# Kernel optimization log

Hardware: AMD Instinct MI355X
Metric: run time of the kernel (lower is better)

The kernel has to match this reference:

```python
import jax, jax.numpy as jnp
import numpy as np


def setup_inputs() -> dict:
    key = jax.random.key(0)
    k1, k2, k3 = jax.random.split(key, 3)
    V, B, L = 512, 256, 40
    seq = jax.random.randint(k1, (B, L), 0, V, dtype=jnp.int32)
    sim_mat = jax.random.normal(k2, (V, V), dtype=jnp.float32)
    pers_mat = jax.random.normal(k3, (V, V, V), dtype=jnp.float32)
    weights = jnp.ones((2,), dtype=jnp.float32)
    return {"seq": seq, "sim_mat": sim_mat, "pers_mat": pers_mat, "weights": weights}


def reference(seq, sim_mat, pers_mat, weights):
    # seq: [B, L] int indices into the V unique responses
    B, L = seq.shape
    V = sim_mat.shape[0]
    # Step 0: uniform log_softmax over V ones -> nll = log(V) per sequence
    nll0 = jnp.float32(B) * jnp.log(jnp.float32(V))
    # Steps t >= 1: logits[b,t] = w0 * sim_mat[seq[b,t-1]] (+ w1 * pers_mat[seq[b,t-2], seq[b,t-1]] for t >= 2)
    prev = seq[:, : L - 1]              # [B, L-1]
    targets = seq[:, 1:]                # [B, L-1]
    logits = weights[0] * sim_mat[prev]                          # [B, L-1, V]
    pers_rows = pers_mat[seq[:, : L - 2], seq[:, 1 : L - 1]]     # [B, L-2, V]
    logits = logits.at[:, 1:, :].add(weights[1] * pers_rows)
    logp = jax.nn.log_softmax(logits, axis=-1)
    nll = -jnp.take_along_axis(logp, targets[..., None], axis=-1).sum()
    return nll0 + nll
```

## Files before the change

### kernel.cpp

```cpp
#include <hip/hip_runtime.h>

constexpr int V = 512;
constexpr int B = 256;
constexpr int L = 40;
constexpr int ROWS = B * (L - 1);
constexpr int WAVES_PER_BLOCK = 4;
constexpr int BLOCKS = 624;
constexpr int TOTAL_WAVES = BLOCKS * WAVES_PER_BLOCK;

__global__ __launch_bounds__(256)
void pers_nll_kernel(const int* __restrict__ seq,
                     const float* __restrict__ sim,
                     const float* __restrict__ pers,
                     const float* __restrict__ wts,
                     float* __restrict__ out)
{
    const int lane        = threadIdx.x & 63;
    const int waveInBlock = threadIdx.x >> 6;
    const int w           = blockIdx.x * WAVES_PER_BLOCK + waveInBlock;

    const float w0 = wts[0];
    const float w1 = wts[1];

    float acc = 0.0f;

    for (int r = w; r < ROWS; r += TOTAL_WAVES) {
        const int b = r / (L - 1);
        const int t = r - b * (L - 1);
        const int prev = seq[b * L + t];
        const int tgt  = seq[b * L + t + 1];

        const int base = lane * 8;
        const float4 s0 = *reinterpret_cast<const float4*>(sim + (size_t)prev * V + base);
        const float4 s1 = *reinterpret_cast<const float4*>(sim + (size_t)prev * V + base + 4);

        float v[8] = { s0.x, s0.y, s0.z, s0.w, s1.x, s1.y, s1.z, s1.w };
        #pragma unroll
        for (int j = 0; j < 8; ++j) v[j] *= w0;

        if (t >= 1) {
            const int p0 = seq[b * L + t - 1];
            const size_t prow = ((size_t)p0 * V + (size_t)prev) * (size_t)V;
            const float4 q0 = *reinterpret_cast<const float4*>(pers + prow + base);
            const float4 q1 = *reinterpret_cast<const float4*>(pers + prow + base + 4);
            v[0] = fmaf(w1, q0.x, v[0]); v[1] = fmaf(w1, q0.y, v[1]);
            v[2] = fmaf(w1, q0.z, v[2]); v[3] = fmaf(w1, q0.w, v[3]);
            v[4] = fmaf(w1, q1.x, v[4]); v[5] = fmaf(w1, q1.y, v[5]);
            v[6] = fmaf(w1, q1.z, v[6]); v[7] = fmaf(w1, q1.w, v[7]);
        }

        float m = v[0];
        #pragma unroll
        for (int j = 1; j < 8; ++j) m = fmaxf(m, v[j]);
        #pragma unroll
        for (int off = 32; off >= 1; off >>= 1)
            m = fmaxf(m, __shfl_xor(m, off, 64));

        float s = 0.0f;
        #pragma unroll
        for (int j = 0; j < 8; ++j) s += __expf(v[j] - m);
        #pragma unroll
        for (int off = 32; off >= 1; off >>= 1)
            s += __shfl_xor(s, off, 64);

        const float cand = v[tgt & 7];
        const float lt   = __shfl(cand, tgt >> 3, 64);

        acc += m + __logf(s) - lt;
    }

    __shared__ float part[WAVES_PER_BLOCK];
    if (lane == 0) part[waveInBlock] = acc;
    __syncthreads();
    if (threadIdx.x == 0) {
        float total = part[0] + part[1] + part[2] + part[3];
        if (blockIdx.x == 0) total += (float)B * logf((float)V);
        atomicAdd(out, total);
    }
}

extern "C" void kernel_launch(void* const* d_in, const int* in_sizes, int n_in,
                              void* d_out, int out_size, void* d_ws, size_t ws_size,
                              hipStream_t stream)
{
    const int*   seq  = (const int*)d_in[0];
    const float* sim  = (const float*)d_in[1];
    const float* pers = (const float*)d_in[2];
    const float* wts  = (const float*)d_in[3];
    float* out = (float*)d_out;

    hipMemsetAsync(out, 0, sizeof(float), stream);
    pers_nll_kernel<<<BLOCKS, 256, 0, stream>>>(seq, sim, pers, wts, out);
}
```

Before: 584.1 us.

## Batch gathered row loads per wave and replace atomic reduction with two-pass sum

Each wave now owns a fixed timestep and processes ITERS rows. All sequence indices and all sim/pers row gathers for those rows are issued up front, so many memory requests are in flight at once instead of one per loop iteration. The t>=1 branch becomes wave-uniform. The memset and the global atomic are replaced by per-block partials in the workspace plus a one-block final reduction kernel. In exchange it adds a second kernel launch and raises register pressure, and it relies on ROWS dividing evenly by TOTAL_WAVES.

```diff
diff --git a/kernel.cpp b/kernel.cpp
--- a/kernel.cpp
+++ b/kernel.cpp
@@ -4,79 +4,117 @@
 constexpr int B = 256;
 constexpr int L = 40;
 constexpr int ROWS = B * (L - 1);
-constexpr int WAVES_PER_BLOCK = 4;
+constexpr int WPB = 4;
 constexpr int BLOCKS = 624;
-constexpr int TOTAL_WAVES = BLOCKS * WAVES_PER_BLOCK;
+constexpr int TOTAL_WAVES = BLOCKS * WPB;
+constexpr int ITERS = ROWS / TOTAL_WAVES;
+
 
 __global__ __launch_bounds__(256)
-void pers_nll_kernel(const int* __restrict__ seq,
-                     const float* __restrict__ sim,
-                     const float* __restrict__ pers,
-                     const float* __restrict__ wts,
-                     float* __restrict__ out)
+void nll_main(const int* __restrict__ seq,
+              const float* __restrict__ sim,
+              const float* __restrict__ pers,
+              const float* __restrict__ wts,
+              float* __restrict__ partial)
 {
-    const int lane        = threadIdx.x & 63;
-    const int waveInBlock = threadIdx.x >> 6;
-    const int w           = blockIdx.x * WAVES_PER_BLOCK + waveInBlock;
+    const int lane = threadIdx.x & 63;
+    const int wib  = threadIdx.x >> 6;
+    const int w    = blockIdx.x * WPB + wib;
 
     const float w0 = wts[0];
     const float w1 = wts[1];
 
+    const int t  = w % 39;
+    const int b0 = w / 39;
+    const int base = lane * 8;
+
+    int prevI[ITERS], tgtI[ITERS], p0I[ITERS];
+    #pragma unroll
+    for (int k = 0; k < ITERS; ++k) {
+        const int off = (b0 + 64 * k) * L + t;
+        prevI[k] = seq[off];
+        tgtI[k]  = seq[off + 1];
+        p0I[k]   = (t >= 1) ? seq[off - 1] : 0;
+    }
+
+    float v[ITERS][8];
+    if (t >= 1) {
+        #pragma unroll
+        for (int k = 0; k < ITERS; ++k) {
+            const float* srow = sim + (size_t)prevI[k] * V + base;
+            const float* prow = pers + ((size_t)p0I[k] * V + (size_t)prevI[k]) * V + base;
+            const float4 s0 = *(const float4*)(srow);
+            const float4 s1 = *(const float4*)(srow + 4);
+            const float4 q0 = *(const float4*)(prow);
+            const float4 q1 = *(const float4*)(prow + 4);
+            v[k][0] = fmaf(w1, q0.x, w0 * s0.x);
+            v[k][1] = fmaf(w1, q0.y, w0 * s0.y);
+            v[k][2] = fmaf(w1, q0.z, w0 * s0.z);
+            v[k][3] = fmaf(w1, q0.w, w0 * s0.w);
+            v[k][4] = fmaf(w1, q1.x, w0 * s1.x);
+            v[k][5] = fmaf(w1, q1.y, w0 * s1.y);
+            v[k][6] = fmaf(w1, q1.z, w0 * s1.z);
+            v[k][7] = fmaf(w1, q1.w, w0 * s1.w);
+        }
+    } else {
+        #pragma unroll
+        for (int k = 0; k < ITERS; ++k) {
+            const float* srow = sim + (size_t)prevI[k] * V + base;
+            const float4 s0 = *(const float4*)(srow);
+            const float4 s1 = *(const float4*)(srow + 4);
+            v[k][0] = w0 * s0.x; v[k][1] = w0 * s0.y;
+            v[k][2] = w0 * s0.z; v[k][3] = w0 * s0.w;
+            v[k][4] = w0 * s1.x; v[k][5] = w0 * s1.y;
+            v[k][6] = w0 * s1.z; v[k][7] = w0 * s1.w;
+        }
+    }
+
     float acc = 0.0f;
-
-    for (int r = w; r < ROWS; r += TOTAL_WAVES) {
-        const int b = r / (L - 1);
-        const int t = r - b * (L - 1);
-        const int prev = seq[b * L + t];
-        const int tgt  = seq[b * L + t + 1];
-
-        const int base = lane * 8;
-        const float4 s0 = *reinterpret_cast<const float4*>(sim + (size_t)prev * V + base);
-        const float4 s1 = *reinterpret_cast<const float4*>(sim + (size_t)prev * V + base + 4);
-
-        float v[8] = { s0.x, s0.y, s0.z, s0.w, s1.x, s1.y, s1.z, s1.w };
+    #pragma unroll
+    for (int k = 0; k < ITERS; ++k) {
+        float m = v[k][0];
         #pragma unroll
-        for (int j = 0; j < 8; ++j) v[j] *= w0;
-
-        if (t >= 1) {
-            const int p0 = seq[b * L + t - 1];
-            const size_t prow = ((size_t)p0 * V + (size_t)prev) * (size_t)V;
-            const float4 q0 = *reinterpret_cast<const float4*>(pers + prow + base);
-            const float4 q1 = *reinterpret_cast<const float4*>(pers + prow + base + 4);
-            v[0] = fmaf(w1, q0.x, v[0]); v[1] = fmaf(w1, q0.y, v[1]);
-            v[2] = fmaf(w1, q0.z, v[2]); v[3] = fmaf(w1, q0.w, v[3]);
-            v[4] = fmaf(w1, q1.x, v[4]); v[5] = fmaf(w1, q1.y, v[5]);
-            v[6] = fmaf(w1, q1.z, v[6]); v[7] = fmaf(w1, q1.w, v[7]);
-        }
-
-        float m = v[0];
-        #pragma unroll
-        for (int j = 1; j < 8; ++j) m = fmaxf(m, v[j]);
+        for (int j = 1; j < 8; ++j) m = fmaxf(m, v[k][j]);
         #pragma unroll
         for (int off = 32; off >= 1; off >>= 1)
             m = fmaxf(m, __shfl_xor(m, off, 64));
 
         float s = 0.0f;
         #pragma unroll
-        for (int j = 0; j < 8; ++j) s += __expf(v[j] - m);
+        for (int j = 0; j < 8; ++j) s += __expf(v[k][j] - m);
         #pragma unroll
         for (int off = 32; off >= 1; off >>= 1)
             s += __shfl_xor(s, off, 64);
 
-        const float cand = v[tgt & 7];
-        const float lt   = __shfl(cand, tgt >> 3, 64);
+        const float cand = v[k][tgtI[k] & 7];
+        const float lt   = __shfl(cand, tgtI[k] >> 3, 64);
 
         acc += m + __logf(s) - lt;
     }
 
-    __shared__ float part[WAVES_PER_BLOCK];
-    if (lane == 0) part[waveInBlock] = acc;
+    __shared__ float part[WPB];
+    if (lane == 0) part[wib] = acc;
     __syncthreads();
-    if (threadIdx.x == 0) {
-        float total = part[0] + part[1] + part[2] + part[3];
-        if (blockIdx.x == 0) total += (float)B * logf((float)V);
-        atomicAdd(out, total);
-    }
+    if (threadIdx.x == 0)
+        partial[blockIdx.x] = part[0] + part[1] + part[2] + part[3];
+}
+
+__global__ __launch_bounds__(256)
+void nll_final(const float* __restrict__ partial, float* __restrict__ out)
+{
+    float s = 0.0f;
+    for (int i = threadIdx.x; i < BLOCKS; i += 256) s += partial[i];
+    #pragma unroll
+    for (int off = 32; off >= 1; off >>= 1) s += __shfl_xor(s, off, 64);
+
+    __shared__ float wsum[4];
+    const int lane = threadIdx.x & 63;
+    const int wib  = threadIdx.x >> 6;
+    if (lane == 0) wsum[wib] = s;
+    __syncthreads();
+    if (threadIdx.x == 0)
+        out[0] = wsum[0] + wsum[1] + wsum[2] + wsum[3]
+               + (float)B * logf((float)V);
 }
 
 extern "C" void kernel_launch(void* const* d_in, const int* in_sizes, int n_in,
@@ -87,8 +125,9 @@
     const float* sim  = (const float*)d_in[1];
     const float* pers = (const float*)d_in[2];
     const float* wts  = (const float*)d_in[3];
-    float* out = (float*)d_out;
+    float* partial = (float*)d_ws;
+    float* out     = (float*)d_out;
 
-    hipMemsetAsync(out, 0, sizeof(float), stream);
-    pers_nll_kernel<<<BLOCKS, 256, 0, stream>>>(seq, sim, pers, wts, out);
+    nll_main<<<BLOCKS, 256, 0, stream>>>(seq, sim, pers, wts, partial);
+    nll_final<<<1, 256, 0, stream>>>(partial, out);
 }
```

Result: no change. 578.7 us (-0.9%).
